# Performance work log

Hardware: AMD Instinct MI355X
Metric: run time of the kernel (lower is better)

Reference implementation:

```python
import jax, jax.numpy as jnp
import numpy as np

# kernel / loss hyperparameters (from base_params)
FIT_SIGMA = 1.0
FIT_L = 1.0
MMD_SIGMA = 1.0
MMD_L = 2.0
REG_LAMBDA = 0.01

N, D = 8192, 16


def setup_inputs() -> dict:
    key = jax.random.key(0)
    k1, k2, k3 = jax.random.split(key, 3)
    X = jax.random.normal(k1, (N, D), dtype=jnp.float32)
    Y = jax.random.normal(k2, (N, D), dtype=jnp.float32)
    Lam = jax.random.normal(k3, (N, D), dtype=jnp.float32)  # nn.init.normal_ on zeros(N,d)
    return {"X": X, "Y": Y, "Lam": Lam}


def _rbf_gram(X, sigma, l):
    # k(xi, xj) = sigma^2 * exp(-||xi - xj||^2 / (2 l^2)), vectorized over all pairs
    sq = jnp.sum(X * X, axis=1)                      # [N]
    d2 = sq[:, None] + sq[None, :] - 2.0 * (X @ X.T)  # [N, N] squared distances
    d2 = jnp.maximum(d2, 0.0)
    return (sigma ** 2) * jnp.exp(-d2 / (2.0 * l ** 2))


def reference(X, Y, Lam):
    fit_kXX = _rbf_gram(X, FIT_SIGMA, FIT_L)   # [N, N]
    mmd_kXX = _rbf_gram(X, MMD_SIGMA, MMD_L)   # [N, N]
    diff = fit_kXX @ Lam - Y                   # [N, d]
    # trace(diff^T K diff) = sum(diff * (K @ diff))
    loss_fit = jnp.sum(diff * (mmd_kXX @ diff))
    loss_reg = REG_LAMBDA * jnp.sum(Lam * (fit_kXX @ Lam))
    return loss_fit + loss_reg
```

## Files before the change

### kernel.cpp

```cpp
#include <hip/hip_runtime.h>

#define NPTS 8192
#define DIM  16
#define DPAD 32

constexpr int BLK = 256;
constexpr int NIB = NPTS / BLK;

#define REG_LAMBDA 0.01f
#define C1 1.2011224087864498f
#define C2 0.6005612043932249f

typedef _Float16 h4 __attribute__((ext_vector_type(4)));
typedef _Float16 h8 __attribute__((ext_vector_type(8)));
typedef float    f4 __attribute__((ext_vector_type(4)));

#define MFMA16(a, b, c) __builtin_amdgcn_mfma_f32_16x16x16f16((a), (b), (c), 0, 0, 0)
#define MFMA32(a, b, c) __builtin_amdgcn_mfma_f32_16x16x32_f16((a), (b), (c), 0, 0, 0)

#if __has_builtin(__builtin_amdgcn_exp2f)
#define EXP2(x) __builtin_amdgcn_exp2f(x)
#else
#define EXP2(x) exp2f(x)
#endif

__device__ __forceinline__ float block_sum(float v, float* wbuf) {
#pragma unroll
  for (int o = 32; o > 0; o >>= 1) v += __shfl_down(v, o, 64);
  const int lane = threadIdx.x & 63;
  const int wid  = threadIdx.x >> 6;
  __syncthreads();
  if (lane == 0) wbuf[wid] = v;
  __syncthreads();
  float s = 0.f;
  if (threadIdx.x == 0) {
#pragma unroll
    for (int w = 0; w < BLK / 64; ++w) s += wbuf[w];
  }
  return s;
}

__global__ __launch_bounds__(BLK) void k_prep(
    const float4* __restrict__ Xv, const float4* __restrict__ Lv,
    _Float16* __restrict__ XA1, _Float16* __restrict__ XB1,
    _Float16* __restrict__ XA2, _Float16* __restrict__ XB2,
    _Float16* __restrict__ LamB, float* __restrict__ accums) {
  if (blockIdx.x == 0 && threadIdx.x < 4) accums[threadIdx.x] = 0.f;
  const int i = blockIdx.x * BLK + threadIdx.x;
  float sq1 = 0.f, sq2 = 0.f;
  h4 a1[4], a2[4];
#pragma unroll
  for (int q = 0; q < 4; ++q) {
    const float4 v = Xv[(size_t)i * 4 + q];
    h4 a = {(_Float16)(C1 * v.x), (_Float16)(C1 * v.y),
            (_Float16)(C1 * v.z), (_Float16)(C1 * v.w)};
    h4 b = {(_Float16)(C2 * v.x), (_Float16)(C2 * v.y),
            (_Float16)(C2 * v.z), (_Float16)(C2 * v.w)};
    a1[q] = a; a2[q] = b;
#pragma unroll
    for (int t = 0; t < 4; ++t) {
      const float fa = (float)a[t], fb = (float)b[t];
      sq1 = fmaf(fa, fa, sq1);
      sq2 = fmaf(fb, fb, sq2);
    }
  }
  const float c1 = -0.5f * sq1, c2 = -0.5f * sq2;
  const _Float16 c1h = (_Float16)c1;
  const _Float16 c1l = (_Float16)(c1 - (float)c1h);
  const _Float16 c2h = (_Float16)c2;
  const _Float16 c2l = (_Float16)(c2 - (float)c2h);
  const _Float16 one = (_Float16)1.f;
  const _Float16 zer = (_Float16)0.f;
  const h4 z4 = {zer, zer, zer, zer};

  h4* rA1 = (h4*)(XA1 + (size_t)i * DPAD);
  h4* rB1 = (h4*)(XB1 + (size_t)i * DPAD);
  h4* rA2 = (h4*)(XA2 + (size_t)i * DPAD);
  h4* rB2 = (h4*)(XB2 + (size_t)i * DPAD);
#pragma unroll
  for (int q = 0; q < 4; ++q) {
    rA1[q] = a1[q]; rB1[q] = a1[q];
    rA2[q] = a2[q]; rB2[q] = a2[q];
  }
  const h4 padA1 = {one, one, c1h, c1l};
  const h4 padB1 = {c1h, c1l, one, one};
  const h4 padA2 = {one, one, c2h, c2l};
  const h4 padB2 = {c2h, c2l, one, one};
  rA1[4] = padA1; rB1[4] = padB1;
  rA2[4] = padA2; rB2[4] = padB2;
#pragma unroll
  for (int q = 5; q < 8; ++q) {
    rA1[q] = z4; rB1[q] = z4; rA2[q] = z4; rB2[q] = z4;
  }

  _Float16* lb = LamB + (size_t)(i >> 4) * 256 + ((i >> 2) & 3) * 64 + (i & 3);
#pragma unroll
  for (int q = 0; q < 4; ++q) {
    const float4 l = Lv[(size_t)i * 4 + q];
    lb[(4 * q + 0) * 4] = (_Float16)l.x;
    lb[(4 * q + 1) * 4] = (_Float16)l.y;
    lb[(4 * q + 2) * 4] = (_Float16)l.z;
    lb[(4 * q + 3) * 4] = (_Float16)l.w;
  }
}

__global__ __launch_bounds__(BLK) void k_pass1(
    const _Float16* __restrict__ XA1, const _Float16* __restrict__ XB1,
    const _Float16* __restrict__ LamB, _Float16* __restrict__ Upart, int span) {
  const int lane = threadIdx.x & 63;
  const int w    = threadIdx.x >> 6;
  const int l16  = lane & 15;
  const int quad = lane >> 4;

  const int i0 = blockIdx.x * 256 + w * 64;
  h8 bxi[4];
#pragma unroll
  for (int t = 0; t < 4; ++t)
    bxi[t] = *(const h8*)(XB1 + (size_t)(i0 + 16 * t + l16) * DPAD + quad * 8);

  const f4 fz = {0.f, 0.f, 0.f, 0.f};
  f4 U[4] = {fz, fz, fz, fz};
  const int jbeg = blockIdx.y * span;
  const int jend = jbeg + span;
#pragma unroll 4
  for (int j0 = jbeg; j0 < jend; j0 += 16) {
    const h8 axj = *(const h8*)(XA1 + (size_t)(j0 + l16) * DPAD + quad * 8);
    const h4 bl  = *(const h4*)(LamB + (size_t)(j0 >> 4) * 256 + lane * 4);
#pragma unroll
    for (int t = 0; t < 4; ++t) {
      const f4 p = MFMA32(axj, bxi[t], fz);
      const auto lo = __builtin_amdgcn_cvt_pkrtz(EXP2(p[0]), EXP2(p[1]));
      const auto hi = __builtin_amdgcn_cvt_pkrtz(EXP2(p[2]), EXP2(p[3]));
      h4 ap;
      ap[0] = lo[0]; ap[1] = lo[1]; ap[2] = hi[0]; ap[3] = hi[1];
      U[t] = MFMA16(ap, bl, U[t]);
    }
  }

  _Float16* dst = Upart + ((size_t)blockIdx.y * NPTS + i0) * DIM;
#pragma unroll
  for (int t = 0; t < 4; ++t)
#pragma unroll
    for (int r = 0; r < 4; ++r)
      dst[(16 * t + quad * 4 + r) * DIM + l16] = (_Float16)U[t][r];
}

__global__ __launch_bounds__(BLK) void k_reduce(
    const _Float16* __restrict__ Upart, const float4* __restrict__ Yv,
    const float4* __restrict__ Lv, _Float16* __restrict__ Dh,
    float* __restrict__ accums, int jc) {
  __shared__ float wred[BLK / 64];
  const int t = blockIdx.x * BLK + threadIdx.x;
  const int i = t >> 1, hf = t & 1;
  float u[8] = {0.f, 0.f, 0.f, 0.f, 0.f, 0.f, 0.f, 0.f};
  for (int c = 0; c < jc; ++c) {
    const h8 p = *(const h8*)(Upart + ((size_t)c * NPTS + i) * DIM + hf * 8);
#pragma unroll
    for (int r = 0; r < 8; ++r) u[r] += (float)p[r];
  }
  const float4 y0 = Yv[(size_t)i * 4 + 2 * hf];
  const float4 y1 = Yv[(size_t)i * 4 + 2 * hf + 1];
  h8 d;
  d[0] = (_Float16)(u[0] - y0.x); d[1] = (_Float16)(u[1] - y0.y);
  d[2] = (_Float16)(u[2] - y0.z); d[3] = (_Float16)(u[3] - y0.w);
  d[4] = (_Float16)(u[4] - y1.x); d[5] = (_Float16)(u[5] - y1.y);
  d[6] = (_Float16)(u[6] - y1.z); d[7] = (_Float16)(u[7] - y1.w);
  *(h8*)(Dh + (size_t)i * DIM + hf * 8) = d;
  const float4 l0 = Lv[(size_t)i * 4 + 2 * hf];
  const float4 l1 = Lv[(size_t)i * 4 + 2 * hf + 1];
  float regp = 0.f;
  regp = fmaf(l0.x, u[0], regp); regp = fmaf(l0.y, u[1], regp);
  regp = fmaf(l0.z, u[2], regp); regp = fmaf(l0.w, u[3], regp);
  regp = fmaf(l1.x, u[4], regp); regp = fmaf(l1.y, u[5], regp);
  regp = fmaf(l1.z, u[6], regp); regp = fmaf(l1.w, u[7], regp);
  const float rtot = block_sum(regp, wred);
  if (threadIdx.x == 0) unsafeAtomicAdd(&accums[1], rtot);
}

__global__ __launch_bounds__(BLK) void k_pass2(
    const _Float16* __restrict__ XA2, const _Float16* __restrict__ XB2,
    const _Float16* __restrict__ Dh, float* __restrict__ accums) {
  __shared__ float wred[BLK / 64];
  const int bi   = blockIdx.x;
  const int k    = blockIdx.y >> 1;
  const int half = blockIdx.y & 1;
  if (k == 16 && bi >= 16) return;
  const int bj = (bi + k) & 31;
  const float weight = (k == 0) ? 1.f : 2.f;

  const int lane = threadIdx.x & 63;
  const int w    = threadIdx.x >> 6;
  const int l16  = lane & 15;
  const int quad = lane >> 4;
  const f4 fz = {0.f, 0.f, 0.f, 0.f};

  const int i0 = bi * 256 + w * 64;
  h8 ax[4];
  h4 ad[4];
#pragma unroll
  for (int t = 0; t < 4; ++t) {
    ax[t] = *(const h8*)(XA2 + (size_t)(i0 + 16 * t + l16) * DPAD + quad * 8);
    ad[t] = *(const h4*)(Dh  + (size_t)(i0 + 16 * t + l16) * DIM + quad * 4);
  }

  float s = 0.f;
  const int jbeg = bj * 256 + half * 128;
  const int jend = jbeg + 128;
#pragma unroll 4
  for (int j0 = jbeg; j0 < jend; j0 += 16) {
    const h8 bx = *(const h8*)(XB2 + (size_t)(j0 + l16) * DPAD + quad * 8);
    const h4 bd = *(const h4*)(Dh  + (size_t)(j0 + l16) * DIM + quad * 4);
#pragma unroll
    for (int t = 0; t < 4; ++t) {
      const f4 dx = MFMA32(ax[t], bx, fz);
      const f4 dd = MFMA16(ad[t], bd, fz);
#pragma unroll
      for (int r = 0; r < 4; ++r) s = fmaf(EXP2(dx[r]), dd[r], s);
    }
  }

  const float stot = block_sum(s * weight, wred);
  if (threadIdx.x == 0) unsafeAtomicAdd(&accums[0], stot);
}

__global__ void k_final(const float* __restrict__ accums, float* __restrict__ out) {
  out[0] = accums[0] + REG_LAMBDA * accums[1];
}

extern "C" void kernel_launch(void* const* d_in, const int* in_sizes, int n_in,
                              void* d_out, int out_size, void* d_ws, size_t ws_size,
                              hipStream_t stream) {
  const float4* Xv = (const float4*)d_in[0];
  const float4* Yv = (const float4*)d_in[1];
  const float4* Lv = (const float4*)d_in[2];
  float* out = (float*)d_out;

  char* base = (char*)d_ws;
  _Float16* XA1  = (_Float16*)(base);
  _Float16* XB1  = (_Float16*)(base + 512 * 1024);
  _Float16* XA2  = (_Float16*)(base + 1024 * 1024);
  _Float16* XB2  = (_Float16*)(base + 1536 * 1024);
  _Float16* LamB = (_Float16*)(base + 2048 * 1024);
  _Float16* Dh   = (_Float16*)(base + 2304 * 1024);
  float*    accums = (float*)(base + 2560 * 1024);
  _Float16* Upart  = (_Float16*)(base + 2560 * 1024 + 256);
  const size_t fixed = 2560 * 1024 + 256;

  int jc = 32;
  while (jc > 1 && fixed + (size_t)jc * NPTS * DIM * 2 > ws_size) jc >>= 1;
  const int span1 = NPTS / jc;

  k_prep<<<NIB, BLK, 0, stream>>>(Xv, Lv, XA1, XB1, XA2, XB2, LamB, accums);
  k_pass1<<<dim3(NPTS / 256, jc), BLK, 0, stream>>>(XA1, XB1, LamB, Upart, span1);
  k_reduce<<<NPTS * 2 / BLK, BLK, 0, stream>>>(Upart, Yv, Lv, Dh, accums, jc);
  k_pass2<<<dim3(32, 34), BLK, 0, stream>>>(XA2, XB2, Dh, accums);
  k_final<<<1, 1, 0, stream>>>(accums, out);
}
```

Measured before the change: 111.6 us.

## Fold final kernel into pass2 via done-counter and spread prep/reduce threads

Removes the separate k_final launch. k_pass2 gains an extra grid row in which one spinning block waits on an atomic done counter and then writes the output. k_prep and k_reduce now use four threads per point instead of one or two, which raises parallelism and makes each thread's memory accesses smaller. The spinning block relies on forward progress of the other blocks, and the counter shares the accumulator slots that k_prep zeroes.

```diff
diff --git a/kernel.cpp b/kernel.cpp
--- a/kernel.cpp
+++ b/kernel.cpp
@@ -5,11 +5,11 @@
 #define DPAD 32
 
 constexpr int BLK = 256;
-constexpr int NIB = NPTS / BLK;
 
 #define REG_LAMBDA 0.01f
 #define C1 1.2011224087864498f
 #define C2 0.6005612043932249f
+#define DONE_TARGET (32 * 34)
 
 typedef _Float16 h4 __attribute__((ext_vector_type(4)));
 typedef _Float16 h8 __attribute__((ext_vector_type(8)));
@@ -23,6 +23,10 @@
 #else
 #define EXP2(x) exp2f(x)
 #endif
+
+__device__ __forceinline__ float dot4(float4 a, float4 b) {
+  return fmaf(a.x, b.x, fmaf(a.y, b.y, fmaf(a.z, b.z, a.w * b.w)));
+}
 
 __device__ __forceinline__ float block_sum(float v, float* wbuf) {
 #pragma unroll
@@ -46,24 +50,24 @@
     _Float16* __restrict__ XA2, _Float16* __restrict__ XB2,
     _Float16* __restrict__ LamB, float* __restrict__ accums) {
   if (blockIdx.x == 0 && threadIdx.x < 4) accums[threadIdx.x] = 0.f;
-  const int i = blockIdx.x * BLK + threadIdx.x;
+  const int t = blockIdx.x * BLK + threadIdx.x;
+  const int i = t >> 2, q = t & 3;
+
+  const float4 v = Xv[(size_t)i * 4 + q];
+  const h4 a = {(_Float16)(C1 * v.x), (_Float16)(C1 * v.y),
+                (_Float16)(C1 * v.z), (_Float16)(C1 * v.w)};
+  const h4 b = {(_Float16)(C2 * v.x), (_Float16)(C2 * v.y),
+                (_Float16)(C2 * v.z), (_Float16)(C2 * v.w)};
   float sq1 = 0.f, sq2 = 0.f;
-  h4 a1[4], a2[4];
-#pragma unroll
-  for (int q = 0; q < 4; ++q) {
-    const float4 v = Xv[(size_t)i * 4 + q];
-    h4 a = {(_Float16)(C1 * v.x), (_Float16)(C1 * v.y),
-            (_Float16)(C1 * v.z), (_Float16)(C1 * v.w)};
-    h4 b = {(_Float16)(C2 * v.x), (_Float16)(C2 * v.y),
-            (_Float16)(C2 * v.z), (_Float16)(C2 * v.w)};
-    a1[q] = a; a2[q] = b;
-#pragma unroll
-    for (int t = 0; t < 4; ++t) {
-      const float fa = (float)a[t], fb = (float)b[t];
-      sq1 = fmaf(fa, fa, sq1);
-      sq2 = fmaf(fb, fb, sq2);
-    }
-  }
+#pragma unroll
+  for (int r = 0; r < 4; ++r) {
+    const float fa = (float)a[r], fb = (float)b[r];
+    sq1 = fmaf(fa, fa, sq1);
+    sq2 = fmaf(fb, fb, sq2);
+  }
+  sq1 += __shfl_xor(sq1, 1, 64); sq1 += __shfl_xor(sq1, 2, 64);
+  sq2 += __shfl_xor(sq2, 1, 64); sq2 += __shfl_xor(sq2, 2, 64);
+
   const float c1 = -0.5f * sq1, c2 = -0.5f * sq2;
   const _Float16 c1h = (_Float16)c1;
   const _Float16 c1l = (_Float16)(c1 - (float)c1h);
@@ -72,36 +76,27 @@
   const _Float16 one = (_Float16)1.f;
   const _Float16 zer = (_Float16)0.f;
   const h4 z4 = {zer, zer, zer, zer};
+  const h4 padA1 = {one, one, c1h, c1l};
+  const h4 padB1 = {c1h, c1l, one, one};
+  const h4 padA2 = {one, one, c2h, c2l};
+  const h4 padB2 = {c2h, c2l, one, one};
 
   h4* rA1 = (h4*)(XA1 + (size_t)i * DPAD);
   h4* rB1 = (h4*)(XB1 + (size_t)i * DPAD);
   h4* rA2 = (h4*)(XA2 + (size_t)i * DPAD);
   h4* rB2 = (h4*)(XB2 + (size_t)i * DPAD);
-#pragma unroll
-  for (int q = 0; q < 4; ++q) {
-    rA1[q] = a1[q]; rB1[q] = a1[q];
-    rA2[q] = a2[q]; rB2[q] = a2[q];
-  }
-  const h4 padA1 = {one, one, c1h, c1l};
-  const h4 padB1 = {c1h, c1l, one, one};
-  const h4 padA2 = {one, one, c2h, c2l};
-  const h4 padB2 = {c2h, c2l, one, one};
-  rA1[4] = padA1; rB1[4] = padB1;
-  rA2[4] = padA2; rB2[4] = padB2;
-#pragma unroll
-  for (int q = 5; q < 8; ++q) {
-    rA1[q] = z4; rB1[q] = z4; rA2[q] = z4; rB2[q] = z4;
-  }
+  rA1[q] = a; rB1[q] = a; rA2[q] = b; rB2[q] = b;
+  rA1[4 + q] = (q == 0) ? padA1 : z4;
+  rB1[4 + q] = (q == 0) ? padB1 : z4;
+  rA2[4 + q] = (q == 0) ? padA2 : z4;
+  rB2[4 + q] = (q == 0) ? padB2 : z4;
 
   _Float16* lb = LamB + (size_t)(i >> 4) * 256 + ((i >> 2) & 3) * 64 + (i & 3);
-#pragma unroll
-  for (int q = 0; q < 4; ++q) {
-    const float4 l = Lv[(size_t)i * 4 + q];
-    lb[(4 * q + 0) * 4] = (_Float16)l.x;
-    lb[(4 * q + 1) * 4] = (_Float16)l.y;
-    lb[(4 * q + 2) * 4] = (_Float16)l.z;
-    lb[(4 * q + 3) * 4] = (_Float16)l.w;
-  }
+  const float4 l = Lv[(size_t)i * 4 + q];
+  lb[(4 * q + 0) * 4] = (_Float16)l.x;
+  lb[(4 * q + 1) * 4] = (_Float16)l.y;
+  lb[(4 * q + 2) * 4] = (_Float16)l.z;
+  lb[(4 * q + 3) * 4] = (_Float16)l.w;
 }
 
 __global__ __launch_bounds__(BLK) void k_pass1(
@@ -151,40 +146,50 @@
     float* __restrict__ accums, int jc) {
   __shared__ float wred[BLK / 64];
   const int t = blockIdx.x * BLK + threadIdx.x;
-  const int i = t >> 1, hf = t & 1;
-  float u[8] = {0.f, 0.f, 0.f, 0.f, 0.f, 0.f, 0.f, 0.f};
+  const int i = t >> 2, q = t & 3;
+  float u0 = 0.f, u1 = 0.f, u2 = 0.f, u3 = 0.f;
   for (int c = 0; c < jc; ++c) {
-    const h8 p = *(const h8*)(Upart + ((size_t)c * NPTS + i) * DIM + hf * 8);
-#pragma unroll
-    for (int r = 0; r < 8; ++r) u[r] += (float)p[r];
-  }
-  const float4 y0 = Yv[(size_t)i * 4 + 2 * hf];
-  const float4 y1 = Yv[(size_t)i * 4 + 2 * hf + 1];
-  h8 d;
-  d[0] = (_Float16)(u[0] - y0.x); d[1] = (_Float16)(u[1] - y0.y);
-  d[2] = (_Float16)(u[2] - y0.z); d[3] = (_Float16)(u[3] - y0.w);
-  d[4] = (_Float16)(u[4] - y1.x); d[5] = (_Float16)(u[5] - y1.y);
-  d[6] = (_Float16)(u[6] - y1.z); d[7] = (_Float16)(u[7] - y1.w);
-  *(h8*)(Dh + (size_t)i * DIM + hf * 8) = d;
-  const float4 l0 = Lv[(size_t)i * 4 + 2 * hf];
-  const float4 l1 = Lv[(size_t)i * 4 + 2 * hf + 1];
-  float regp = 0.f;
-  regp = fmaf(l0.x, u[0], regp); regp = fmaf(l0.y, u[1], regp);
-  regp = fmaf(l0.z, u[2], regp); regp = fmaf(l0.w, u[3], regp);
-  regp = fmaf(l1.x, u[4], regp); regp = fmaf(l1.y, u[5], regp);
-  regp = fmaf(l1.z, u[6], regp); regp = fmaf(l1.w, u[7], regp);
+    const h4 p = *(const h4*)(Upart + ((size_t)c * NPTS + i) * DIM + q * 4);
+    u0 += (float)p[0]; u1 += (float)p[1];
+    u2 += (float)p[2]; u3 += (float)p[3];
+  }
+  const float4 y = Yv[(size_t)i * 4 + q];
+  const h4 d = {(_Float16)(u0 - y.x), (_Float16)(u1 - y.y),
+                (_Float16)(u2 - y.z), (_Float16)(u3 - y.w)};
+  *(h4*)(Dh + (size_t)i * DIM + q * 4) = d;
+  const float4 uu = {u0, u1, u2, u3};
+  const float regp = dot4(Lv[(size_t)i * 4 + q], uu);
   const float rtot = block_sum(regp, wred);
   if (threadIdx.x == 0) unsafeAtomicAdd(&accums[1], rtot);
 }
 
 __global__ __launch_bounds__(BLK) void k_pass2(
     const _Float16* __restrict__ XA2, const _Float16* __restrict__ XB2,
-    const _Float16* __restrict__ Dh, float* __restrict__ accums) {
+    const _Float16* __restrict__ Dh, float* __restrict__ accums,
+    float* __restrict__ out) {
+  int* done = (int*)(accums + 2);
+  if (blockIdx.y == 34) {
+    if (blockIdx.x != 0 || threadIdx.x != 0) return;
+    while (__hip_atomic_load(done, __ATOMIC_ACQUIRE, __HIP_MEMORY_SCOPE_AGENT)
+           < DONE_TARGET)
+      __builtin_amdgcn_s_sleep(2);
+    const float a0 = __hip_atomic_load(accums + 0, __ATOMIC_RELAXED,
+                                       __HIP_MEMORY_SCOPE_AGENT);
+    const float a1 = __hip_atomic_load(accums + 1, __ATOMIC_RELAXED,
+                                       __HIP_MEMORY_SCOPE_AGENT);
+    out[0] = a0 + REG_LAMBDA * a1;
+    return;
+  }
+
   __shared__ float wred[BLK / 64];
   const int bi   = blockIdx.x;
   const int k    = blockIdx.y >> 1;
   const int half = blockIdx.y & 1;
-  if (k == 16 && bi >= 16) return;
+  if (k == 16 && bi >= 16) {
+    if (threadIdx.x == 0)
+      __hip_atomic_fetch_add(done, 1, __ATOMIC_RELEASE, __HIP_MEMORY_SCOPE_AGENT);
+    return;
+  }
   const int bj = (bi + k) & 31;
   const float weight = (k == 0) ? 1.f : 2.f;
 
@@ -220,11 +225,10 @@
   }
 
   const float stot = block_sum(s * weight, wred);
-  if (threadIdx.x == 0) unsafeAtomicAdd(&accums[0], stot);
-}
-
-__global__ void k_final(const float* __restrict__ accums, float* __restrict__ out) {
-  out[0] = accums[0] + REG_LAMBDA * accums[1];
+  if (threadIdx.x == 0) {
+    unsafeAtomicAdd(&accums[0], stot);
+    __hip_atomic_fetch_add(done, 1, __ATOMIC_RELEASE, __HIP_MEMORY_SCOPE_AGENT);
+  }
 }
 
 extern "C" void kernel_launch(void* const* d_in, const int* in_sizes, int n_in,
@@ -250,9 +254,8 @@
   while (jc > 1 && fixed + (size_t)jc * NPTS * DIM * 2 > ws_size) jc >>= 1;
   const int span1 = NPTS / jc;
 
-  k_prep<<<NIB, BLK, 0, stream>>>(Xv, Lv, XA1, XB1, XA2, XB2, LamB, accums);
+  k_prep<<<NPTS * 4 / BLK, BLK, 0, stream>>>(Xv, Lv, XA1, XB1, XA2, XB2, LamB, accums);
   k_pass1<<<dim3(NPTS / 256, jc), BLK, 0, stream>>>(XA1, XB1, LamB, Upart, span1);
-  k_reduce<<<NPTS * 2 / BLK, BLK, 0, stream>>>(Upart, Yv, Lv, Dh, accums, jc);
-  k_pass2<<<dim3(32, 34), BLK, 0, stream>>>(XA2, XB2, Dh, accums);
-  k_final<<<1, 1, 0, stream>>>(accums, out);
-}
+  k_reduce<<<NPTS * 4 / BLK, BLK, 0, stream>>>(Upart, Yv, Lv, Dh, accums, jc);
+  k_pass2<<<dim3(32, 35), BLK, 0, stream>>>(XA2, XB2, Dh, accums, out);
+}
```

Result: slower. 122.2 us (+9.5%).
